# Kernel tuning notes

Hardware: AMD Instinct MI355X
Metric: run time of the kernel (lower is better)

The kernel has to match this reference:

```python
import jax, jax.numpy as jnp
import numpy as np

B, S_STATE, S_SEQ, H = 64, 512, 2048, 512


def setup_inputs() -> dict:
    key = jax.random.key(0)
    k1, k2, k3, k4 = jax.random.split(key, 4)
    out_state = jax.random.normal(k1, (B, S_STATE, H), dtype=jnp.float32)
    history = jax.random.normal(k2, (B, S_SEQ, H), dtype=jnp.float32)
    # nn.Linear(hidden, hidden): weight [H, H], bias [H]
    bound = 1.0 / np.sqrt(H)
    attn_w = jax.random.uniform(k3, (H, H), minval=-bound, maxval=bound, dtype=jnp.float32)
    attn_b = jax.random.uniform(k4, (H,), minval=-bound, maxval=bound, dtype=jnp.float32)
    return {"out_state": out_state, "history": history, "attn_w": attn_w, "attn_b": attn_b}


def reference(out_state, history, attn_w, attn_b):
    # method == 'general': energy[k,i,j] = out_state[k,i] . (W @ history[k,j] + b)
    proj = jnp.einsum('bjd,hd->bjh', history, attn_w) + attn_b  # [B, S_SEQ, H]
    energies = jnp.einsum('bih,bjh->bij', out_state, proj)      # [B, S_STATE, S_SEQ]
    return jax.nn.softmax(energies, axis=2)
```

## Files before the change

### kernel.cpp

```cpp
#include <hip/hip_runtime.h>
#include <math.h>

constexpr int B        = 64;
constexpr int S_STATE  = 512;
constexpr int S_SEQ    = 2048;
constexpr int H        = 512;

typedef __attribute__((ext_vector_type(8))) short bf16x8;
typedef __attribute__((ext_vector_type(4))) float f32x4;

static __device__ __forceinline__ unsigned short f2bf(float f) {
    unsigned int u = __float_as_uint(f);
    u = u + 0x7FFFu + ((u >> 16) & 1u);
    return (unsigned short)(u >> 16);
}
static __device__ __forceinline__ float bf2f(unsigned short h) {
    return __uint_as_float(((unsigned int)h) << 16);
}

static __device__ __forceinline__ unsigned pack_hi16(unsigned b0, unsigned b1) {
    return __builtin_amdgcn_perm(b1, b0, 0x07060302u);
}

static __device__ __forceinline__ void split8(const float4 x, const float4 y,
                                              uint4& hi, uint4& lo) {
    const unsigned b0 = __float_as_uint(x.x), b1 = __float_as_uint(x.y);
    const unsigned b2 = __float_as_uint(x.z), b3 = __float_as_uint(x.w);
    const unsigned b4 = __float_as_uint(y.x), b5 = __float_as_uint(y.y);
    const unsigned b6 = __float_as_uint(y.z), b7 = __float_as_uint(y.w);
    hi.x = pack_hi16(b0, b1);
    hi.y = pack_hi16(b2, b3);
    hi.z = pack_hi16(b4, b5);
    hi.w = pack_hi16(b6, b7);
    const float r0 = x.x - __uint_as_float(b0 & 0xFFFF0000u);
    const float r1 = x.y - __uint_as_float(b1 & 0xFFFF0000u);
    const float r2 = x.z - __uint_as_float(b2 & 0xFFFF0000u);
    const float r3 = x.w - __uint_as_float(b3 & 0xFFFF0000u);
    const float r4 = y.x - __uint_as_float(b4 & 0xFFFF0000u);
    const float r5 = y.y - __uint_as_float(b5 & 0xFFFF0000u);
    const float r6 = y.z - __uint_as_float(b6 & 0xFFFF0000u);
    const float r7 = y.w - __uint_as_float(b7 & 0xFFFF0000u);
    lo.x = pack_hi16(__float_as_uint(r0), __float_as_uint(r1));
    lo.y = pack_hi16(__float_as_uint(r2), __float_as_uint(r3));
    lo.z = pack_hi16(__float_as_uint(r4), __float_as_uint(r5));
    lo.w = pack_hi16(__float_as_uint(r6), __float_as_uint(r7));
}

__global__ __launch_bounds__(256) void split_transpose_w(const float* __restrict__ w,
                                                         unsigned short* __restrict__ thi,
                                                         unsigned short* __restrict__ tlo) {
    int idx = blockIdx.x * 256 + threadIdx.x;
    int h = idx >> 9, d = idx & 511;
    float v = w[idx];
    unsigned short hh = f2bf(v);
    thi[d * 512 + h] = hh;
    tlo[d * 512 + h] = f2bf(v - bf2f(hh));
}

constexpr int LP = 40;

template <bool A_F32, bool B_F32, bool SPLIT_OUT>
__global__ __launch_bounds__(256)
void gemm_nt_mfma(const float* __restrict__ Af,
                  const unsigned short* __restrict__ Ahi, const unsigned short* __restrict__ Alo,
                  const float* __restrict__ Bf,
                  const unsigned short* __restrict__ Bhi, const unsigned short* __restrict__ Blo,
                  float* __restrict__ Cf, unsigned short* __restrict__ Chi,
                  unsigned short* __restrict__ Clo,
                  int K, int N, size_t aBatch, size_t bBatch, size_t cBatch) {
    __shared__ unsigned short sA[2][128 * LP];
    __shared__ unsigned short sB[2][128 * LP];

    const int t = threadIdx.x;

    unsigned bx = blockIdx.x, by = blockIdx.y, bz = blockIdx.z;
    {
        const unsigned gx = gridDim.x, gxy = gridDim.x * gridDim.y;
        const unsigned total = gxy * gridDim.z;
        if ((total & 7u) == 0u) {
            const unsigned lid = bx + gx * by + gxy * bz;
            const unsigned swz = (lid & 7u) * (total >> 3) + (lid >> 3);
            bz = swz / gxy;
            const unsigned rem = swz - bz * gxy;
            by = rem / gx;
            bx = rem - by * gx;
        }
    }

    const int m0 = by * 128;
    const int n0 = bx * 128;
    const size_t aOff = (size_t)bz * aBatch;
    const size_t bOff = (size_t)bz * bBatch;
    const size_t cOff = (size_t)bz * cBatch;

    const int lane = t & 63, wv = t >> 6;
    const int wm = wv >> 1, wn = wv & 1;
    const int lrow = lane & 15, quad = lane >> 4;
    const int fko = quad * 8;

    const int r0 = t >> 2;
    const int kk = (t & 3) * 8;

    f32x4 acc[4][4];
#pragma unroll
    for (int i = 0; i < 4; ++i)
#pragma unroll
        for (int j = 0; j < 4; ++j) acc[i][j] = (f32x4){0.f, 0.f, 0.f, 0.f};

    for (int k0 = 0; k0 < K; k0 += 32) {
        uint4 vAh0, vAh1, vAl0, vAl1, vBh0, vBh1, vBl0, vBl1;
        {
            const size_t ga0 = aOff + (size_t)(m0 + r0) * K + k0 + kk;
            const size_t ga1 = ga0 + (size_t)64 * K;
            if constexpr (A_F32) {
                const float4 x0 = *reinterpret_cast<const float4*>(&Af[ga0]);
                const float4 x1 = *reinterpret_cast<const float4*>(&Af[ga0 + 4]);
                const float4 y0 = *reinterpret_cast<const float4*>(&Af[ga1]);
                const float4 y1 = *reinterpret_cast<const float4*>(&Af[ga1 + 4]);
                split8(x0, x1, vAh0, vAl0);
                split8(y0, y1, vAh1, vAl1);
            } else {
                vAh0 = *reinterpret_cast<const uint4*>(&Ahi[ga0]);
                vAh1 = *reinterpret_cast<const uint4*>(&Ahi[ga1]);
                vAl0 = *reinterpret_cast<const uint4*>(&Alo[ga0]);
                vAl1 = *reinterpret_cast<const uint4*>(&Alo[ga1]);
            }
        }
        {
            const size_t gb0 = bOff + (size_t)(n0 + r0) * K + k0 + kk;
            const size_t gb1 = gb0 + (size_t)64 * K;
            if constexpr (B_F32) {
                const float4 x0 = *reinterpret_cast<const float4*>(&Bf[gb0]);
                const float4 x1 = *reinterpret_cast<const float4*>(&Bf[gb0 + 4]);
                const float4 y0 = *reinterpret_cast<const float4*>(&Bf[gb1]);
                const float4 y1 = *reinterpret_cast<const float4*>(&Bf[gb1 + 4]);
                split8(x0, x1, vBh0, vBl0);
                split8(y0, y1, vBh1, vBl1);
            } else {
                vBh0 = *reinterpret_cast<const uint4*>(&Bhi[gb0]);
                vBh1 = *reinterpret_cast<const uint4*>(&Bhi[gb1]);
                vBl0 = *reinterpret_cast<const uint4*>(&Blo[gb0]);
                vBl1 = *reinterpret_cast<const uint4*>(&Blo[gb1]);
            }
        }

        __syncthreads();
        const int s0 = r0 * LP + kk, s1 = (r0 + 64) * LP + kk;
        *reinterpret_cast<uint4*>(&sA[0][s0]) = vAh0;
        *reinterpret_cast<uint4*>(&sA[0][s1]) = vAh1;
        *reinterpret_cast<uint4*>(&sA[1][s0]) = vAl0;
        *reinterpret_cast<uint4*>(&sA[1][s1]) = vAl1;
        *reinterpret_cast<uint4*>(&sB[0][s0]) = vBh0;
        *reinterpret_cast<uint4*>(&sB[0][s1]) = vBh1;
        *reinterpret_cast<uint4*>(&sB[1][s0]) = vBl0;
        *reinterpret_cast<uint4*>(&sB[1][s1]) = vBl1;
        __syncthreads();

        bf16x8 aH[4], aL[4];
#pragma unroll
        for (int mt = 0; mt < 4; ++mt) {
            const int r = (wm * 64 + mt * 16 + lrow) * LP + fko;
            aH[mt] = *reinterpret_cast<const bf16x8*>(&sA[0][r]);
            aL[mt] = *reinterpret_cast<const bf16x8*>(&sA[1][r]);
        }
#pragma unroll
        for (int nt = 0; nt < 4; ++nt) {
            const int r = (wn * 64 + nt * 16 + lrow) * LP + fko;
            const bf16x8 bH = *reinterpret_cast<const bf16x8*>(&sB[0][r]);
            const bf16x8 bL = *reinterpret_cast<const bf16x8*>(&sB[1][r]);
#pragma unroll
            for (int mt = 0; mt < 4; ++mt) {
                acc[mt][nt] = __builtin_amdgcn_mfma_f32_16x16x32_bf16(aH[mt], bH, acc[mt][nt], 0, 0, 0);
                acc[mt][nt] = __builtin_amdgcn_mfma_f32_16x16x32_bf16(aH[mt], bL, acc[mt][nt], 0, 0, 0);
                acc[mt][nt] = __builtin_amdgcn_mfma_f32_16x16x32_bf16(aL[mt], bH, acc[mt][nt], 0, 0, 0);
            }
        }
    }

#pragma unroll
    for (int mt = 0; mt < 4; ++mt) {
#pragma unroll
        for (int nt = 0; nt < 4; ++nt) {
#pragma unroll
            for (int r = 0; r < 4; ++r) {
                const int gi = m0 + wm * 64 + mt * 16 + quad * 4 + r;
                const int gj = n0 + wn * 64 + nt * 16 + lrow;
                const float v = acc[mt][nt][r];
                if constexpr (SPLIT_OUT) {
                    const unsigned short hh = f2bf(v);
                    Chi[cOff + (size_t)gi * N + gj] = hh;
                    Clo[cOff + (size_t)gi * N + gj] = f2bf(v - bf2f(hh));
                } else {
                    Cf[cOff + (size_t)gi * N + gj] = v;
                }
            }
        }
    }
}

__global__ __launch_bounds__(256) void softmax_rows(float* __restrict__ out) {
    const int t = threadIdx.x;
    const size_t base = (size_t)blockIdx.x * S_SEQ;

    float4 v0 = *reinterpret_cast<float4*>(&out[base + (t << 2)]);
    float4 v1 = *reinterpret_cast<float4*>(&out[base + 1024 + (t << 2)]);

    float m = fmaxf(fmaxf(fmaxf(v0.x, v0.y), fmaxf(v0.z, v0.w)),
                    fmaxf(fmaxf(v1.x, v1.y), fmaxf(v1.z, v1.w)));
#pragma unroll
    for (int off = 32; off; off >>= 1) m = fmaxf(m, __shfl_xor(m, off));

    __shared__ float redm[4];
    __shared__ float reds[4];
    if ((t & 63) == 0) redm[t >> 6] = m;
    __syncthreads();
    m = fmaxf(fmaxf(redm[0], redm[1]), fmaxf(redm[2], redm[3]));

    v0.x = __expf(v0.x - m); v0.y = __expf(v0.y - m);
    v0.z = __expf(v0.z - m); v0.w = __expf(v0.w - m);
    v1.x = __expf(v1.x - m); v1.y = __expf(v1.y - m);
    v1.z = __expf(v1.z - m); v1.w = __expf(v1.w - m);

    float s = v0.x + v0.y + v0.z + v0.w + v1.x + v1.y + v1.z + v1.w;
#pragma unroll
    for (int off = 32; off; off >>= 1) s += __shfl_xor(s, off);
    if ((t & 63) == 0) reds[t >> 6] = s;
    __syncthreads();
    s = reds[0] + reds[1] + reds[2] + reds[3];

    const float inv = 1.0f / s;
    v0.x *= inv; v0.y *= inv; v0.z *= inv; v0.w *= inv;
    v1.x *= inv; v1.y *= inv; v1.z *= inv; v1.w *= inv;

    *reinterpret_cast<float4*>(&out[base + (t << 2)]) = v0;
    *reinterpret_cast<float4*>(&out[base + 1024 + (t << 2)]) = v1;
}

__global__ __launch_bounds__(256) void gemm_nn(const float* __restrict__ A,
                                               const float* __restrict__ Bg,
                                               float* __restrict__ C) {
    constexpr int K = H, N = H;
    __shared__ float As[32][68];
    __shared__ float Bs[32][68];
    const int t  = threadIdx.x;
    const int m0 = blockIdx.y * 64;
    const int n0 = blockIdx.x * 64;
    const int aK = (t & 7) << 2;
    const int aR = t >> 3;
    const int bN = (t & 15) << 2;
    const int bK = t >> 4;
    const int tx = t & 15;
    const int ty = t >> 4;
    float acc[4][4];
#pragma unroll
    for (int i = 0; i < 4; ++i)
#pragma unroll
        for (int j = 0; j < 4; ++j) acc[i][j] = 0.f;
    for (int k0 = 0; k0 < K; k0 += 32) {
#pragma unroll
        for (int r = 0; r < 2; ++r) {
            const int row = aR + 32 * r;
            const float4 v = *reinterpret_cast<const float4*>(&A[(size_t)(m0 + row) * K + k0 + aK]);
            As[aK + 0][row] = v.x; As[aK + 1][row] = v.y;
            As[aK + 2][row] = v.z; As[aK + 3][row] = v.w;
        }
#pragma unroll
        for (int r = 0; r < 2; ++r) {
            const int kkk = bK + 16 * r;
            *reinterpret_cast<float4*>(&Bs[kkk][bN]) =
                *reinterpret_cast<const float4*>(&Bg[(size_t)(k0 + kkk) * N + n0 + bN]);
        }
        __syncthreads();
#pragma unroll
        for (int kkk = 0; kkk < 32; ++kkk) {
            const float4 av = *reinterpret_cast<const float4*>(&As[kkk][ty << 2]);
            const float4 bv = *reinterpret_cast<const float4*>(&Bs[kkk][tx << 2]);
            const float a[4] = {av.x, av.y, av.z, av.w};
            const float b[4] = {bv.x, bv.y, bv.z, bv.w};
#pragma unroll
            for (int i = 0; i < 4; ++i)
#pragma unroll
                for (int j = 0; j < 4; ++j) acc[i][j] += a[i] * b[j];
        }
        __syncthreads();
    }
#pragma unroll
    for (int i = 0; i < 4; ++i) {
        float4 v = make_float4(acc[i][0], acc[i][1], acc[i][2], acc[i][3]);
        *reinterpret_cast<float4*>(&C[(size_t)(m0 + (ty << 2) + i) * N + n0 + (tx << 2)]) = v;
    }
}

__global__ __launch_bounds__(256) void gemm_nt_batched(const float* __restrict__ Q,
                                                       const float* __restrict__ Hist,
                                                       float* __restrict__ E) {
    constexpr int K = H;
    __shared__ float As[32][68];
    __shared__ float Bs[32][68];
    const int t  = threadIdx.x;
    const int m0 = blockIdx.y * 64;
    const int n0 = blockIdx.x * 64;
    const int b  = blockIdx.z;
    const float* Qb = Q    + (size_t)b * S_STATE * H;
    const float* Hb = Hist + (size_t)b * S_SEQ   * H;
    float*       Eb = E    + (size_t)b * S_STATE * S_SEQ;
    const int aK = (t & 7) << 2;
    const int aR = t >> 3;
    const int tx = t & 15;
    const int ty = t >> 4;
    float acc[4][4];
#pragma unroll
    for (int i = 0; i < 4; ++i)
#pragma unroll
        for (int j = 0; j < 4; ++j) acc[i][j] = 0.f;
    for (int k0 = 0; k0 < K; k0 += 32) {
#pragma unroll
        for (int r = 0; r < 2; ++r) {
            const int row = aR + 32 * r;
            const float4 v = *reinterpret_cast<const float4*>(&Qb[(size_t)(m0 + row) * K + k0 + aK]);
            As[aK + 0][row] = v.x; As[aK + 1][row] = v.y;
            As[aK + 2][row] = v.z; As[aK + 3][row] = v.w;
        }
#pragma unroll
        for (int r = 0; r < 2; ++r) {
            const int row = aR + 32 * r;
            const float4 v = *reinterpret_cast<const float4*>(&Hb[(size_t)(n0 + row) * K + k0 + aK]);
            Bs[aK + 0][row] = v.x; Bs[aK + 1][row] = v.y;
            Bs[aK + 2][row] = v.z; Bs[aK + 3][row] = v.w;
        }
        __syncthreads();
#pragma unroll
        for (int kkk = 0; kkk < 32; ++kkk) {
            const float4 av = *reinterpret_cast<const float4*>(&As[kkk][ty << 2]);
            const float4 bv = *reinterpret_cast<const float4*>(&Bs[kkk][tx << 2]);
            const float a[4] = {av.x, av.y, av.z, av.w};
            const float b2[4] = {bv.x, bv.y, bv.z, bv.w};
#pragma unroll
            for (int i = 0; i < 4; ++i)
#pragma unroll
                for (int j = 0; j < 4; ++j) acc[i][j] += a[i] * b2[j];
        }
        __syncthreads();
    }
#pragma unroll
    for (int i = 0; i < 4; ++i) {
        float4 v = make_float4(acc[i][0], acc[i][1], acc[i][2], acc[i][3]);
        *reinterpret_cast<float4*>(&Eb[(size_t)(m0 + (ty << 2) + i) * S_SEQ + n0 + (tx << 2)]) = v;
    }
}

extern "C" void kernel_launch(void* const* d_in, const int* in_sizes, int n_in,
                              void* d_out, int out_size, void* d_ws, size_t ws_size,
                              hipStream_t stream) {
    const float* out_state = (const float*)d_in[0];
    const float* history   = (const float*)d_in[1];
    const float* attn_w    = (const float*)d_in[2];
    float* out = (float*)d_out;

    const size_t nOS = (size_t)B * S_STATE * H;
    const size_t nW  = (size_t)H * H;
    size_t off = 0;
    auto alloc = [&](size_t bytes) { size_t o = off; off = (off + bytes + 255) & ~(size_t)255; return o; };
    char* ws = (char*)d_ws;
    const size_t o_wth = alloc(nW * 2),  o_wtl = alloc(nW * 2);
    const size_t o_qh  = alloc(nOS * 2), o_ql  = alloc(nOS * 2);
    const size_t need = off;

    if (ws_size >= need) {
        unsigned short* wt_h = (unsigned short*)(ws + o_wth);
        unsigned short* wt_l = (unsigned short*)(ws + o_wtl);
        unsigned short* q_h  = (unsigned short*)(ws + o_qh);
        unsigned short* q_l  = (unsigned short*)(ws + o_ql);

        split_transpose_w<<<(int)(nW / 256), 256, 0, stream>>>(attn_w, wt_h, wt_l);

        gemm_nt_mfma<true, false, true><<<dim3(H / 128, (B * S_STATE) / 128, 1), 256, 0, stream>>>(
            out_state, nullptr, nullptr, nullptr, wt_h, wt_l,
            nullptr, q_h, q_l, H, H, 0, 0, 0);

        gemm_nt_mfma<false, true, false><<<dim3(S_SEQ / 128, S_STATE / 128, B), 256, 0, stream>>>(
            nullptr, q_h, q_l, history, nullptr, nullptr,
            out, nullptr, nullptr, H, S_SEQ,
            (size_t)S_STATE * H, (size_t)S_SEQ * H, (size_t)S_STATE * S_SEQ);

        softmax_rows<<<B * S_STATE, 256, 0, stream>>>(out);
    } else {
        float* q = (float*)d_ws;
        gemm_nn<<<dim3(H / 64, (B * S_STATE) / 64), 256, 0, stream>>>(out_state, attn_w, q);
        gemm_nt_batched<<<dim3(S_SEQ / 64, S_STATE / 64, B), 256, 0, stream>>>(q, history, out);
        softmax_rows<<<B * S_STATE, 256, 0, stream>>>(out);
    }
}
```

Before: 750.2 us.

## Prefetch next K tile, pack hi/lo bf16 pairs, and use warp-per-row softmax

The MFMA GEMM loop now issues global loads for the next K-slice right after the shared-memory stores, so they overlap with the current slice's MFMAs. The hi/lo bf16 split buffers are packed into one 32-bit word per element and unpacked with byte-perm instructions, and a launch-bounds occupancy hint of 3 is added. Softmax now gives each 64-lane wave a whole row, which removes the shared-memory reductions and block barriers. In exchange, the held prefetch registers may raise register pressure, and the occupancy hint may cause spills.

```diff
diff --git a/kernel.cpp b/kernel.cpp
--- a/kernel.cpp
+++ b/kernel.cpp
@@ -20,6 +20,9 @@
 
 static __device__ __forceinline__ unsigned pack_hi16(unsigned b0, unsigned b1) {
     return __builtin_amdgcn_perm(b1, b0, 0x07060302u);
+}
+static __device__ __forceinline__ unsigned pack_lo16(unsigned b0, unsigned b1) {
+    return __builtin_amdgcn_perm(b1, b0, 0x05040100u);
 }
 
 static __device__ __forceinline__ void split8(const float4 x, const float4 y,
@@ -46,27 +49,31 @@
     lo.w = pack_hi16(__float_as_uint(r6), __float_as_uint(r7));
 }
 
+static __device__ __forceinline__ void unpack8(const uint4 p0, const uint4 p1,
+                                               uint4& hi, uint4& lo) {
+    hi.x = pack_hi16(p0.x, p0.y); lo.x = pack_lo16(p0.x, p0.y);
+    hi.y = pack_hi16(p0.z, p0.w); lo.y = pack_lo16(p0.z, p0.w);
+    hi.z = pack_hi16(p1.x, p1.y); lo.z = pack_lo16(p1.x, p1.y);
+    hi.w = pack_hi16(p1.z, p1.w); lo.w = pack_lo16(p1.z, p1.w);
+}
+
 __global__ __launch_bounds__(256) void split_transpose_w(const float* __restrict__ w,
-                                                         unsigned short* __restrict__ thi,
-                                                         unsigned short* __restrict__ tlo) {
+                                                         unsigned* __restrict__ thl) {
     int idx = blockIdx.x * 256 + threadIdx.x;
     int h = idx >> 9, d = idx & 511;
     float v = w[idx];
     unsigned short hh = f2bf(v);
-    thi[d * 512 + h] = hh;
-    tlo[d * 512 + h] = f2bf(v - bf2f(hh));
+    unsigned short ll = f2bf(v - bf2f(hh));
+    thl[d * 512 + h] = ((unsigned)hh << 16) | (unsigned)ll;
 }
 
 constexpr int LP = 40;
 
 template <bool A_F32, bool B_F32, bool SPLIT_OUT>
-__global__ __launch_bounds__(256)
-void gemm_nt_mfma(const float* __restrict__ Af,
-                  const unsigned short* __restrict__ Ahi, const unsigned short* __restrict__ Alo,
-                  const float* __restrict__ Bf,
-                  const unsigned short* __restrict__ Bhi, const unsigned short* __restrict__ Blo,
-                  float* __restrict__ Cf, unsigned short* __restrict__ Chi,
-                  unsigned short* __restrict__ Clo,
+__global__ __launch_bounds__(256, 3)
+void gemm_nt_mfma(const float* __restrict__ Af, const unsigned* __restrict__ Apk,
+                  const float* __restrict__ Bf, const unsigned* __restrict__ Bpk,
+                  float* __restrict__ Cf, unsigned* __restrict__ Cpk,
                   int K, int N, size_t aBatch, size_t bBatch, size_t cBatch) {
     __shared__ unsigned short sA[2][128 * LP];
     __shared__ unsigned short sB[2][128 * LP];
@@ -107,43 +114,51 @@
 #pragma unroll
         for (int j = 0; j < 4; ++j) acc[i][j] = (f32x4){0.f, 0.f, 0.f, 0.f};
 
+    uint4 vAh0, vAh1, vAl0, vAl1, vBh0, vBh1, vBl0, vBl1;
+
+    auto loadA = [&](int k0) {
+        const size_t ga0 = aOff + (size_t)(m0 + r0) * K + k0 + kk;
+        const size_t ga1 = ga0 + (size_t)64 * K;
+        if constexpr (A_F32) {
+            const float4 x0 = *reinterpret_cast<const float4*>(&Af[ga0]);
+            const float4 x1 = *reinterpret_cast<const float4*>(&Af[ga0 + 4]);
+            const float4 y0 = *reinterpret_cast<const float4*>(&Af[ga1]);
+            const float4 y1 = *reinterpret_cast<const float4*>(&Af[ga1 + 4]);
+            split8(x0, x1, vAh0, vAl0);
+            split8(y0, y1, vAh1, vAl1);
+        } else {
+            const uint4 p00 = *reinterpret_cast<const uint4*>(&Apk[ga0]);
+            const uint4 p01 = *reinterpret_cast<const uint4*>(&Apk[ga0 + 4]);
+            const uint4 p10 = *reinterpret_cast<const uint4*>(&Apk[ga1]);
+            const uint4 p11 = *reinterpret_cast<const uint4*>(&Apk[ga1 + 4]);
+            unpack8(p00, p01, vAh0, vAl0);
+            unpack8(p10, p11, vAh1, vAl1);
+        }
+    };
+    auto loadB = [&](int k0) {
+        const size_t gb0 = bOff + (size_t)(n0 + r0) * K + k0 + kk;
+        const size_t gb1 = gb0 + (size_t)64 * K;
+        if constexpr (B_F32) {
+            const float4 x0 = *reinterpret_cast<const float4*>(&Bf[gb0]);
+            const float4 x1 = *reinterpret_cast<const float4*>(&Bf[gb0 + 4]);
+            const float4 y0 = *reinterpret_cast<const float4*>(&Bf[gb1]);
+            const float4 y1 = *reinterpret_cast<const float4*>(&Bf[gb1 + 4]);
+            split8(x0, x1, vBh0, vBl0);
+            split8(y0, y1, vBh1, vBl1);
+        } else {
+            const uint4 p00 = *reinterpret_cast<const uint4*>(&Bpk[gb0]);
+            const uint4 p01 = *reinterpret_cast<const uint4*>(&Bpk[gb0 + 4]);
+            const uint4 p10 = *reinterpret_cast<const uint4*>(&Bpk[gb1]);
+            const uint4 p11 = *reinterpret_cast<const uint4*>(&Bpk[gb1 + 4]);
+            unpack8(p00, p01, vBh0, vBl0);
+            unpack8(p10, p11, vBh1, vBl1);
+        }
+    };
+
+    loadA(0);
+    loadB(0);
+
     for (int k0 = 0; k0 < K; k0 += 32) {
-        uint4 vAh0, vAh1, vAl0, vAl1, vBh0, vBh1, vBl0, vBl1;
-        {
-            const size_t ga0 = aOff + (size_t)(m0 + r0) * K + k0 + kk;
-            const size_t ga1 = ga0 + (size_t)64 * K;
-            if constexpr (A_F32) {
-                const float4 x0 = *reinterpret_cast<const float4*>(&Af[ga0]);
-                const float4 x1 = *reinterpret_cast<const float4*>(&Af[ga0 + 4]);
-                const float4 y0 = *reinterpret_cast<const float4*>(&Af[ga1]);
-                const float4 y1 = *reinterpret_cast<const float4*>(&Af[ga1 + 4]);
-                split8(x0, x1, vAh0, vAl0);
-                split8(y0, y1, vAh1, vAl1);
-            } else {
-                vAh0 = *reinterpret_cast<const uint4*>(&Ahi[ga0]);
-                vAh1 = *reinterpret_cast<const uint4*>(&Ahi[ga1]);
-                vAl0 = *reinterpret_cast<const uint4*>(&Alo[ga0]);
-                vAl1 = *reinterpret_cast<const uint4*>(&Alo[ga1]);
-            }
-        }
-        {
-            const size_t gb0 = bOff + (size_t)(n0 + r0) * K + k0 + kk;
-            const size_t gb1 = gb0 + (size_t)64 * K;
-            if constexpr (B_F32) {
-                const float4 x0 = *reinterpret_cast<const float4*>(&Bf[gb0]);
-                const float4 x1 = *reinterpret_cast<const float4*>(&Bf[gb0 + 4]);
-                const float4 y0 = *reinterpret_cast<const float4*>(&Bf[gb1]);
-                const float4 y1 = *reinterpret_cast<const float4*>(&Bf[gb1 + 4]);
-                split8(x0, x1, vBh0, vBl0);
-                split8(y0, y1, vBh1, vBl1);
-            } else {
-                vBh0 = *reinterpret_cast<const uint4*>(&Bhi[gb0]);
-                vBh1 = *reinterpret_cast<const uint4*>(&Bhi[gb1]);
-                vBl0 = *reinterpret_cast<const uint4*>(&Blo[gb0]);
-                vBl1 = *reinterpret_cast<const uint4*>(&Blo[gb1]);
-            }
-        }
-
         __syncthreads();
         const int s0 = r0 * LP + kk, s1 = (r0 + 64) * LP + kk;
         *reinterpret_cast<uint4*>(&sA[0][s0]) = vAh0;
@@ -156,6 +171,11 @@
         *reinterpret_cast<uint4*>(&sB[1][s1]) = vBl1;
         __syncthreads();
 
+        if (k0 + 32 < K) {
+            loadA(k0 + 32);
+            loadB(k0 + 32);
+        }
+
         bf16x8 aH[4], aL[4];
 #pragma unroll
         for (int mt = 0; mt < 4; ++mt) {
@@ -188,8 +208,8 @@
                 const float v = acc[mt][nt][r];
                 if constexpr (SPLIT_OUT) {
                     const unsigned short hh = f2bf(v);
-                    Chi[cOff + (size_t)gi * N + gj] = hh;
-                    Clo[cOff + (size_t)gi * N + gj] = f2bf(v - bf2f(hh));
+                    const unsigned short ll = f2bf(v - bf2f(hh));
+                    Cpk[cOff + (size_t)gi * N + gj] = ((unsigned)hh << 16) | (unsigned)ll;
                 } else {
                     Cf[cOff + (size_t)gi * N + gj] = v;
                 }
@@ -199,41 +219,39 @@
 }
 
 __global__ __launch_bounds__(256) void softmax_rows(float* __restrict__ out) {
-    const int t = threadIdx.x;
-    const size_t base = (size_t)blockIdx.x * S_SEQ;
-
-    float4 v0 = *reinterpret_cast<float4*>(&out[base + (t << 2)]);
-    float4 v1 = *reinterpret_cast<float4*>(&out[base + 1024 + (t << 2)]);
-
-    float m = fmaxf(fmaxf(fmaxf(v0.x, v0.y), fmaxf(v0.z, v0.w)),
-                    fmaxf(fmaxf(v1.x, v1.y), fmaxf(v1.z, v1.w)));
+    const int lane = threadIdx.x & 63;
+    const int wv   = threadIdx.x >> 6;
+    const size_t row  = (size_t)blockIdx.x * 4 + wv;
+    const size_t base = row * S_SEQ + (lane << 2);
+
+    float4 v[8];
+#pragma unroll
+    for (int c = 0; c < 8; ++c)
+        v[c] = *reinterpret_cast<float4*>(&out[base + c * 256]);
+
+    float m = -INFINITY;
+#pragma unroll
+    for (int c = 0; c < 8; ++c)
+        m = fmaxf(m, fmaxf(fmaxf(v[c].x, v[c].y), fmaxf(v[c].z, v[c].w)));
 #pragma unroll
     for (int off = 32; off; off >>= 1) m = fmaxf(m, __shfl_xor(m, off));
 
-    __shared__ float redm[4];
-    __shared__ float reds[4];
-    if ((t & 63) == 0) redm[t >> 6] = m;
-    __syncthreads();
-    m = fmaxf(fmaxf(redm[0], redm[1]), fmaxf(redm[2], redm[3]));
-
-    v0.x = __expf(v0.x - m); v0.y = __expf(v0.y - m);
-    v0.z = __expf(v0.z - m); v0.w = __expf(v0.w - m);
-    v1.x = __expf(v1.x - m); v1.y = __expf(v1.y - m);
-    v1.z = __expf(v1.z - m); v1.w = __expf(v1.w - m);
-
-    float s = v0.x + v0.y + v0.z + v0.w + v1.x + v1.y + v1.z + v1.w;
+    float s = 0.f;
+#pragma unroll
+    for (int c = 0; c < 8; ++c) {
+        v[c].x = __expf(v[c].x - m); v[c].y = __expf(v[c].y - m);
+        v[c].z = __expf(v[c].z - m); v[c].w = __expf(v[c].w - m);
+        s += v[c].x + v[c].y + v[c].z + v[c].w;
+    }
 #pragma unroll
     for (int off = 32; off; off >>= 1) s += __shfl_xor(s, off);
-    if ((t & 63) == 0) reds[t >> 6] = s;
-    __syncthreads();
-    s = reds[0] + reds[1] + reds[2] + reds[3];
 
     const float inv = 1.0f / s;
-    v0.x *= inv; v0.y *= inv; v0.z *= inv; v0.w *= inv;
-    v1.x *= inv; v1.y *= inv; v1.z *= inv; v1.w *= inv;
-
-    *reinterpret_cast<float4*>(&out[base + (t << 2)]) = v0;
-    *reinterpret_cast<float4*>(&out[base + 1024 + (t << 2)]) = v1;
+#pragma unroll
+    for (int c = 0; c < 8; ++c) {
+        v[c].x *= inv; v[c].y *= inv; v[c].z *= inv; v[c].w *= inv;
+        *reinterpret_cast<float4*>(&out[base + c * 256]) = v[c];
+    }
 }
 
 __global__ __launch_bounds__(256) void gemm_nn(const float* __restrict__ A,
@@ -362,32 +380,30 @@
     size_t off = 0;
     auto alloc = [&](size_t bytes) { size_t o = off; off = (off + bytes + 255) & ~(size_t)255; return o; };
     char* ws = (char*)d_ws;
-    const size_t o_wth = alloc(nW * 2),  o_wtl = alloc(nW * 2);
-    const size_t o_qh  = alloc(nOS * 2), o_ql  = alloc(nOS * 2);
+    const size_t o_wt = alloc(nW * 4);
+    const size_t o_q  = alloc(nOS * 4);
     const size_t need = off;
 
     if (ws_size >= need) {
-        unsigned short* wt_h = (unsigned short*)(ws + o_wth);
-        unsigned short* wt_l = (unsigned short*)(ws + o_wtl);
-        unsigned short* q_h  = (unsigned short*)(ws + o_qh);
-        unsigned short* q_l  = (unsigned short*)(ws + o_ql);
-
-        split_transpose_w<<<(int)(nW / 256), 256, 0, stream>>>(attn_w, wt_h, wt_l);
+        unsigned* wt_hl = (unsigned*)(ws + o_wt);
+        unsigned* q_hl  = (unsigned*)(ws + o_q);
+
+        split_transpose_w<<<(int)(nW / 256), 256, 0, stream>>>(attn_w, wt_hl);
 
         gemm_nt_mfma<true, false, true><<<dim3(H / 128, (B * S_STATE) / 128, 1), 256, 0, stream>>>(
-            out_state, nullptr, nullptr, nullptr, wt_h, wt_l,
-            nullptr, q_h, q_l, H, H, 0, 0, 0);
+            out_state, nullptr, nullptr, wt_hl,
+            nullptr, q_hl, H, H, 0, 0, 0);
 
         gemm_nt_mfma<false, true, false><<<dim3(S_SEQ / 128, S_STATE / 128, B), 256, 0, stream>>>(
-            nullptr, q_h, q_l, history, nullptr, nullptr,
-            out, nullptr, nullptr, H, S_SEQ,
+            nullptr, q_hl, history, nullptr,
+            out, nullptr, H, S_SEQ,
             (size_t)S_STATE * H, (size_t)S_SEQ * H, (size_t)S_STATE * S_SEQ);
 
-        softmax_rows<<<B * S_STATE, 256, 0, stream>>>(out);
+        softmax_rows<<<(B * S_STATE) / 4, 256, 0, stream>>>(out);
     } else {
         float* q = (float*)d_ws;
         gemm_nn<<<dim3(H / 64, (B * S_STATE) / 64), 256, 0, stream>>>(out_state, attn_w, q);
         gemm_nt_batched<<<dim3(S_SEQ / 64, S_STATE / 64, B), 256, 0, stream>>>(q, history, out);
-        softmax_rows<<<B * S_STATE, 256, 0, stream>>>(out);
-    }
-}
+        softmax_rows<<<(B * S_STATE) / 4, 256, 0, stream>>>(out);
+    }
+}
```

Measured after the change: 758.0 us. Within noise of the previous version (+1.0%).
